# Kernel optimization log

Measured on AMD Instinct MI355X. Metric: run time of the kernel, lower is better.

## Reference

```python
import jax, jax.numpy as jnp
import numpy as np

# Each of the 16 real-valued binary logic ops is a polynomial
#   c0 + c1*a + c2*b + c3*a*b
# Rows correspond to op_idx 0..15 from bin_op().
_OP_COEFFS = np.array([
    [0.,  0.,  0.,  0.],   # 0: false
    [0.,  0.,  0.,  1.],   # 1: a*b
    [0.,  1.,  0., -1.],   # 2: a*(1-b)
    [0.,  1.,  0.,  0.],   # 3: a
    [0.,  0.,  1., -1.],   # 4: (1-a)*b
    [0.,  0.,  1.,  0.],   # 5: b
    [0.,  1.,  1., -2.],   # 6: xor
    [0.,  1.,  1., -1.],   # 7: or
    [1., -1., -1.,  1.],   # 8: nor
    [1., -1., -1.,  2.],   # 9: xnor
    [1.,  0., -1.,  0.],   # 10: not b
    [1.,  0., -1.,  1.],   # 11: b -> a
    [1., -1.,  0.,  0.],   # 12: not a
    [1., -1.,  0.,  1.],   # 13: a -> b
    [1.,  0.,  0., -1.],   # 14: nand
    [1.,  0.,  0.,  0.],   # 15: true
], dtype=np.float32)

BATCH, IN_DIM, OUT_DIM = 2048, 16384, 16384


def setup_inputs() -> dict:
    key = jax.random.key(0)
    k1, k2, k3, k4 = jax.random.split(key, 4)
    x = jax.random.uniform(k1, (BATCH, IN_DIM), dtype=jnp.float32)
    idx_a = jax.random.randint(k2, (OUT_DIM,), 0, IN_DIM, dtype=jnp.int32)
    idx_b = jax.random.randint(k3, (OUT_DIM,), 0, IN_DIM, dtype=jnp.int32)
    weights = jax.random.normal(k4, (OUT_DIM, 16), dtype=jnp.float32)
    return {"x": x, "idx_a": idx_a, "idx_b": idx_b, "weights": weights}


def reference(x, idx_a, idx_b, weights):
    # gate probabilities over the 16 ops, per output neuron: [out_dim, 16]
    probs = jax.nn.softmax(weights, axis=-1)
    # collapse the 16-way weighted combination into 4 polynomial coeffs
    coef = probs @ jnp.asarray(_OP_COEFFS, dtype=probs.dtype)  # [out_dim, 4]
    a = x[:, idx_a]  # [batch, out_dim]
    b = x[:, idx_b]  # [batch, out_dim]
    out = coef[:, 0] + coef[:, 1] * a + coef[:, 2] * b + coef[:, 3] * (a * b)
    return out
```

## Files before the change

kernel.cpp:

```cpp
#include <hip/hip_runtime.h>
#include <hip/hip_fp16.h>

#define IN_DIM  16384
#define OUT_DIM 16384
#define BATCH   2048
#define TPB     512
#define ITS     (OUT_DIM / (TPB * 4))
#define CHK     (IN_DIM / (TPB * 8))

typedef float f32x4 __attribute__((ext_vector_type(4)));

struct h2x2 { __half2 ab, cd; };

__device__ __constant__ float OPC[16][4] = {
    {0.f, 0.f, 0.f, 0.f}, {0.f, 0.f, 0.f, 1.f}, {0.f, 1.f, 0.f, -1.f}, {0.f, 1.f, 0.f, 0.f},
    {0.f, 0.f, 1.f, -1.f}, {0.f, 0.f, 1.f, 0.f}, {0.f, 1.f, 1.f, -2.f}, {0.f, 1.f, 1.f, -1.f},
    {1.f, -1.f, -1.f, 1.f}, {1.f, -1.f, -1.f, 2.f}, {1.f, 0.f, -1.f, 0.f}, {1.f, 0.f, -1.f, 1.f},
    {1.f, -1.f, 0.f, 0.f}, {1.f, -1.f, 0.f, 1.f}, {1.f, 0.f, 0.f, -1.f}, {1.f, 0.f, 0.f, 0.f}};

__global__ __launch_bounds__(256) void prep_kernel(const float* __restrict__ w,
                                                   const int* __restrict__ ia,
                                                   const int* __restrict__ ib,
                                                   h2x2* __restrict__ coefh,
                                                   unsigned* __restrict__ packed) {
    int j = blockIdx.x * 256 + threadIdx.x;
    if (j >= OUT_DIM) return;

    const float4* wr = (const float4*)(w + (size_t)j * 16);
    float wv[16];
    float4 w0 = wr[0], w1 = wr[1], w2 = wr[2], w3 = wr[3];
    wv[0] = w0.x; wv[1] = w0.y; wv[2] = w0.z; wv[3] = w0.w;
    wv[4] = w1.x; wv[5] = w1.y; wv[6] = w1.z; wv[7] = w1.w;
    wv[8] = w2.x; wv[9] = w2.y; wv[10] = w2.z; wv[11] = w2.w;
    wv[12] = w3.x; wv[13] = w3.y; wv[14] = w3.z; wv[15] = w3.w;

    float m = wv[0];
#pragma unroll
    for (int k = 1; k < 16; ++k) m = fmaxf(m, wv[k]);
    float s = 0.f;
#pragma unroll
    for (int k = 0; k < 16; ++k) { wv[k] = expf(wv[k] - m); s += wv[k]; }
    float inv = 1.f / s;

    float c0 = 0.f, c1 = 0.f, c2 = 0.f, c3 = 0.f;
#pragma unroll
    for (int k = 0; k < 16; ++k) {
        float p = wv[k];
        c0 = fmaf(p, OPC[k][0], c0);
        c1 = fmaf(p, OPC[k][1], c1);
        c2 = fmaf(p, OPC[k][2], c2);
        c3 = fmaf(p, OPC[k][3], c3);
    }
    h2x2 c;
    c.ab = __floats2half2_rn(c0 * inv, c1 * inv);
    c.cd = __floats2half2_rn(c2 * inv, c3 * inv);
    coefh[j] = c;
    packed[j] = ((unsigned)ia[j] << 1) | ((unsigned)ib[j] << 17);
}

__device__ __forceinline__ unsigned pack2(float a, float b) {
    return __builtin_bit_cast(unsigned, __builtin_amdgcn_cvt_pkrtz(a, b));
}

__global__ __launch_bounds__(TPB, 4) void logic_kernel(const float* __restrict__ x,
                                                       const unsigned* __restrict__ packed,
                                                       const h2x2* __restrict__ coefh,
                                                       float* __restrict__ out) {
    __shared__ __half lds[IN_DIM];

    const int tid = threadIdx.x;
    const size_t row = blockIdx.x;

    {
        const float4* s4 = (const float4*)(x + row * IN_DIM);
        uint4 tt[CHK];
#pragma unroll
        for (int c = 0; c < CHK; ++c) {
            float4 v0 = s4[(c * TPB + tid) * 2 + 0];
            float4 v1 = s4[(c * TPB + tid) * 2 + 1];
            tt[c].x = pack2(v0.x, v0.y); tt[c].y = pack2(v0.z, v0.w);
            tt[c].z = pack2(v1.x, v1.y); tt[c].w = pack2(v1.z, v1.w);
        }
#pragma unroll
        for (int c = 0; c < CHK; ++c)
            *(uint4*)((char*)lds + (size_t)(c * TPB + tid) * 16) = tt[c];
    }
    __syncthreads();

    const char* bufc = (const char*)lds;
    float* outr = out + row * IN_DIM;

#pragma unroll
    for (int it = 0; it < ITS; ++it) {
        const int j0 = (it * TPB + tid) * 4;
        const uint4 pi = *(const uint4*)(packed + j0);

        const h2x2 cA = coefh[j0 + 0];
        const h2x2 cB = coefh[j0 + 1];
        const h2x2 cC = coefh[j0 + 2];
        const h2x2 cD = coefh[j0 + 3];

        f32x4 o;
#define COL(P, CF, FLD)                                                             \
        {                                                                           \
            float a = __half2float(*(const __half*)(bufc + ((P) & 0xFFFFu)));       \
            float b = __half2float(*(const __half*)(bufc + ((P) >> 16)));           \
            float c0 = __low2float(CF.ab), c1 = __high2float(CF.ab);                \
            float c2 = __low2float(CF.cd), c3 = __high2float(CF.cd);                \
            o.FLD = fmaf(a, fmaf(c3, b, c1), fmaf(c2, b, c0));                      \
        }
        COL(pi.x, cA, x)
        COL(pi.y, cB, y)
        COL(pi.z, cC, z)
        COL(pi.w, cD, w)
#undef COL
        *(f32x4*)(outr + j0) = o;
    }
}

extern "C" void kernel_launch(void* const* d_in, const int* in_sizes, int n_in,
                              void* d_out, int out_size, void* d_ws, size_t ws_size,
                              hipStream_t stream) {
    const float* x = (const float*)d_in[0];
    const int* ia = (const int*)d_in[1];
    const int* ib = (const int*)d_in[2];
    const float* w = (const float*)d_in[3];
    float* out = (float*)d_out;

    h2x2* coefh = (h2x2*)d_ws;
    unsigned* packed = (unsigned*)((char*)d_ws + (size_t)OUT_DIM * sizeof(h2x2));

    prep_kernel<<<OUT_DIM / 256, 256, 0, stream>>>(w, ia, ib, coefh, packed);
    logic_kernel<<<BATCH, TPB, 0, stream>>>(x, packed, coefh, out);
}
```

Before: 58.68 us.

## Prefetch index/coef metadata before barrier and double-buffer across iterations, 8 outputs per thread

Each thread now handles 8 output columns per iteration instead of 4, halving the iteration count. The packed indices and fp16 coefficients for the first iteration are issued before the LDS barrier, and the next iteration's metadata is prefetched into registers while the current one is computed. The goal is to hide global-load latency for the metadata behind the staging of x and the compute. The cost is higher register pressure, so launch bounds drop to 2 blocks per CU hint, which may reduce occupancy, and each thread's output stores become less coalesced.

```diff
diff --git a/kernel.cpp b/kernel.cpp
--- a/kernel.cpp
+++ b/kernel.cpp
@@ -5,7 +5,7 @@
 #define OUT_DIM 16384
 #define BATCH   2048
 #define TPB     512
-#define ITS     (OUT_DIM / (TPB * 4))
+#define ITS     (OUT_DIM / (TPB * 8))
 #define CHK     (IN_DIM / (TPB * 8))
 
 typedef float f32x4 __attribute__((ext_vector_type(4)));
@@ -62,7 +62,7 @@
     return __builtin_bit_cast(unsigned, __builtin_amdgcn_cvt_pkrtz(a, b));
 }
 
-__global__ __launch_bounds__(TPB, 4) void logic_kernel(const float* __restrict__ x,
+__global__ __launch_bounds__(TPB, 2) void logic_kernel(const float* __restrict__ x,
                                                        const unsigned* __restrict__ packed,
                                                        const h2x2* __restrict__ coefh,
                                                        float* __restrict__ out) {
@@ -85,6 +85,13 @@
         for (int c = 0; c < CHK; ++c)
             *(uint4*)((char*)lds + (size_t)(c * TPB + tid) * 16) = tt[c];
     }
+
+    uint4 p0 = *(const uint4*)(packed + tid * 8);
+    uint4 p1 = *(const uint4*)(packed + tid * 8 + 4);
+    h2x2 cf[8];
+#pragma unroll
+    for (int k = 0; k < 8; ++k) cf[k] = coefh[tid * 8 + k];
+
     __syncthreads();
 
     const char* bufc = (const char*)lds;
@@ -92,29 +99,41 @@
 
 #pragma unroll
     for (int it = 0; it < ITS; ++it) {
-        const int j0 = (it * TPB + tid) * 4;
-        const uint4 pi = *(const uint4*)(packed + j0);
+        const int j0 = (it * TPB + tid) * 8;
 
-        const h2x2 cA = coefh[j0 + 0];
-        const h2x2 cB = coefh[j0 + 1];
-        const h2x2 cC = coefh[j0 + 2];
-        const h2x2 cD = coefh[j0 + 3];
+        const uint4 q0 = p0, q1 = p1;
+        h2x2 cc[8];
+#pragma unroll
+        for (int k = 0; k < 8; ++k) cc[k] = cf[k];
 
-        f32x4 o;
-#define COL(P, CF, FLD)                                                             \
+        if (it + 1 < ITS) {
+            const int jn = ((it + 1) * TPB + tid) * 8;
+            p0 = *(const uint4*)(packed + jn);
+            p1 = *(const uint4*)(packed + jn + 4);
+#pragma unroll
+            for (int k = 0; k < 8; ++k) cf[k] = coefh[jn + k];
+        }
+
+        f32x4 oL, oH;
+#define COL(P, CF, OV, FLD)                                                         \
         {                                                                           \
             float a = __half2float(*(const __half*)(bufc + ((P) & 0xFFFFu)));       \
             float b = __half2float(*(const __half*)(bufc + ((P) >> 16)));           \
-            float c0 = __low2float(CF.ab), c1 = __high2float(CF.ab);                \
-            float c2 = __low2float(CF.cd), c3 = __high2float(CF.cd);                \
-            o.FLD = fmaf(a, fmaf(c3, b, c1), fmaf(c2, b, c0));                      \
+            float c0 = __low2float((CF).ab), c1 = __high2float((CF).ab);            \
+            float c2 = __low2float((CF).cd), c3 = __high2float((CF).cd);            \
+            OV.FLD = fmaf(a, fmaf(c3, b, c1), fmaf(c2, b, c0));                     \
         }
-        COL(pi.x, cA, x)
-        COL(pi.y, cB, y)
-        COL(pi.z, cC, z)
-        COL(pi.w, cD, w)
+        COL(q0.x, cc[0], oL, x)
+        COL(q0.y, cc[1], oL, y)
+        COL(q0.z, cc[2], oL, z)
+        COL(q0.w, cc[3], oL, w)
+        COL(q1.x, cc[4], oH, x)
+        COL(q1.y, cc[5], oH, y)
+        COL(q1.z, cc[6], oH, z)
+        COL(q1.w, cc[7], oH, w)
 #undef COL
-        *(f32x4*)(outr + j0) = o;
+        *(f32x4*)(outr + j0) = oL;
+        *(f32x4*)(outr + j0 + 4) = oH;
     }
 }
 
```

New measurement: 68.28 us. +16.4%, slower.
